# Kernel tuning notes

Hardware: AMD Instinct MI355X
Metric: run time of the kernel (lower is better)

Reference implementation:

```python
import jax, jax.numpy as jnp
import numpy as np

B, N, E = 64, 256, 2048          # graphs per batch, nodes per subgraph, edges per subgraph
V, D, H = 50000, 128, 4          # vocab_size, hidden_dim, heads
NEG_SLOPE = 0.2                  # PyG GATConv default LeakyReLU slope


def setup_inputs() -> dict:
    key = jax.random.key(0)
    ks = jax.random.split(key, 16)
    s = 0.05
    return {
        "neighbors_node1": jax.random.randint(ks[0], (B, N), 0, V),
        "neighbors_node2": jax.random.randint(ks[1], (B, N), 0, V),
        "adj1": jax.random.randint(ks[2], (B, 2, E), 0, N),
        "adj2": jax.random.randint(ks[3], (B, 2, E), 0, N),
        "emb": jax.random.normal(ks[4], (V + 1, D), jnp.float32) * 0.02,
        # GATConv 1: lin weight [H*D, D], att_src/att_dst [H, D], bias [D] (concat=False)
        "W1": jax.random.normal(ks[5], (H * D, D), jnp.float32) * s,
        "att_src1": jax.random.normal(ks[6], (H, D), jnp.float32) * s,
        "att_dst1": jax.random.normal(ks[7], (H, D), jnp.float32) * s,
        "b1": jnp.zeros((D,), jnp.float32),
        # GATConv 2
        "W2": jax.random.normal(ks[8], (H * D, D), jnp.float32) * s,
        "att_src2": jax.random.normal(ks[9], (H, D), jnp.float32) * s,
        "att_dst2": jax.random.normal(ks[10], (H, D), jnp.float32) * s,
        "b2": jnp.zeros((D,), jnp.float32),
        # final MLP: Linear(2D -> 1)
        "mlp_w": jax.random.normal(ks[11], (1, 2 * D), jnp.float32) * s,
        "mlp_b": jnp.zeros((1,), jnp.float32),
    }


def _gat_conv(x, edge_index, W, a_src, a_dst, bias):
    """PyG GATConv, concat=False (mean over heads), with self-loops.
    x: [N, D] node features; edge_index: [2, E] (row=src j, col=dst i)."""
    xh = (x @ W.T).reshape(N, H, D)                      # [N, H, D]
    loop = jnp.arange(N)
    src = jnp.concatenate([edge_index[0], loop])          # [E+N]
    dst = jnp.concatenate([edge_index[1], loop])
    asrc = jnp.einsum('nhd,hd->nh', xh, a_src)            # [N, H]
    adst = jnp.einsum('nhd,hd->nh', xh, a_dst)
    e = jax.nn.leaky_relu(asrc[src] + adst[dst], NEG_SLOPE)   # [E+N, H]
    # softmax over incoming edges of each dst node
    m = jax.ops.segment_max(e, dst, num_segments=N)
    ex = jnp.exp(e - m[dst])
    denom = jax.ops.segment_sum(ex, dst, num_segments=N)
    alpha = ex / denom[dst]                               # [E+N, H]
    out = jax.ops.segment_sum(xh[src] * alpha[:, :, None], dst, num_segments=N)  # [N, H, D]
    return out.mean(axis=1) + bias                        # [N, D]


def reference(neighbors_node1, neighbors_node2, adj1, adj2, emb,
              W1, att_src1, att_dst1, b1,
              W2, att_src2, att_dst2, b2,
              mlp_w, mlp_b):
    f1 = jax.vmap(lambda n, ei: _gat_conv(emb[n], ei, W1, att_src1, att_dst1, b1))(
        neighbors_node1, adj1)                            # [B, N, D]
    f2 = jax.vmap(lambda n, ei: _gat_conv(emb[n], ei, W2, att_src2, att_dst2, b2))(
        neighbors_node2, adj2)
    feats = jnp.concatenate([f1[:, 0], f2[:, 0]], axis=-1)  # center node of each subgraph -> [B, 2D]
    return (feats @ mlp_w.T + mlp_b)[:, 0]                # [B]
```

## Files before the change

kernel.cpp:

```cpp
#include <hip/hip_runtime.h>
#include <hip/hip_bf16.h>

#define Bg 64
#define Nn 256
#define Ee 2048
#define Dd 128
#define Hh 4
#define MAXJ 40
#define RS 132
#define MAGIC 0x13579BDF

__device__ __forceinline__ float loadf(const void* p, long i, int f32) {
    return f32 ? ((const float*)p)[i]
               : __bfloat162float(((const __hip_bfloat16*)p)[i]);
}

__global__ __launch_bounds__(256) void gat_one_kernel(
    const int* nn1, const int* nn2, const int* adj1, const int* adj2,
    const void* emb,
    const void* W1, const void* as1, const void* ad1, const void* b1,
    const void* W2, const void* as2, const void* ad2, const void* b2,
    const void* mlpw, const void* mlpb,
    float* wv,
    int* wvflag,
    float* partial,
    int* pairflag,
    void* out)
{
    __shared__ float s_av[Dd];
    __shared__ float s_wv[12 * RS];
    __shared__ float s_rows[MAXJ * RS];
    __shared__ int   s_srcj[MAXJ];
    __shared__ int   s_gid[MAXJ];
    __shared__ int   s_cnt, s_f32;
    __shared__ float s_ps[MAXJ * Hh], s_pm[MAXJ * Hh];
    __shared__ float s_pd[Hh], s_hval[Hh], s_bd;

    const int tid = threadIdx.x;
    const int x = blockIdx.x;
    const int b = x & (Bg - 1);
    const int l = x >> 6;

    if (tid == 0) { s_f32 = 0; s_cnt = 0; }
    __syncthreads();
    {
        float v = __bfloat162float(((const __hip_bfloat16*)W1)[tid]);
        if (!(v > -64.f && v < 64.f)) atomicOr(&s_f32, 1);
    }
    __syncthreads();
    const int f32 = s_f32;

    if (x < 24) {
        const int h = x & 3, t = (x >> 2) % 3, pl = x / 12;
        const void* avp; long off;
        if (t == 0)      { avp = pl ? as2 : as1; off = (long)h * Dd; }
        else if (t == 1) { avp = pl ? ad2 : ad1; off = (long)h * Dd; }
        else             { avp = mlpw;           off = (long)pl * Dd; }
        if (tid < Dd) s_av[tid] = loadf(avp, off + tid, f32);
        __syncthreads();
        if (tid < Dd) {
            const void* W = pl ? W2 : W1;
            float acc = 0.f;
            if (f32) {
                const float* Wf = (const float*)W + (long)h * Dd * Dd + tid;
                #pragma unroll 8
                for (int d = 0; d < Dd; ++d) acc += s_av[d] * Wf[(long)d * Dd];
            } else {
                const __hip_bfloat16* Wb =
                    (const __hip_bfloat16*)W + (long)h * Dd * Dd + tid;
                #pragma unroll 8
                for (int d = 0; d < Dd; ++d)
                    acc += s_av[d] * __bfloat162float(Wb[(long)d * Dd]);
            }
            __hip_atomic_store(&wv[x * Dd + tid], acc,
                               __ATOMIC_RELAXED, __HIP_MEMORY_SCOPE_AGENT);
        }
        __threadfence();
        __syncthreads();
        if (tid == 0) atomicExch(&wvflag[x], MAGIC);
    } else if (x == 24 || x == 25) {
        const int pl = x - 24;
        if (tid < Dd)
            s_av[tid] = loadf(pl ? b2 : b1, tid, f32) *
                        loadf(mlpw, (long)pl * Dd + tid, f32);
        __syncthreads();
        if (tid == 0) {
            float a = 0.f;
            for (int d = 0; d < Dd; ++d) a += s_av[d];
            if (pl == 0) a += loadf(mlpb, 0, f32);
            __hip_atomic_store(&wv[3072 + pl], a,
                               __ATOMIC_RELAXED, __HIP_MEMORY_SCOPE_AGENT);
            __threadfence();
            atomicExch(&wvflag[24 + pl], MAGIC);
        }
    }

    const int* adjp = (l ? adj2 : adj1) + (long)b * 2 * Ee;
    const int* dstp = adjp + Ee;
    for (int i = tid; i < Ee / 4; i += 256) {
        int4 d4 = ((const int4*)dstp)[i];
        int base = i * 4;
        if (d4.x == 0) { int p = atomicAdd(&s_cnt, 1); if (p < MAXJ - 1) s_srcj[p] = adjp[base + 0]; }
        if (d4.y == 0) { int p = atomicAdd(&s_cnt, 1); if (p < MAXJ - 1) s_srcj[p] = adjp[base + 1]; }
        if (d4.z == 0) { int p = atomicAdd(&s_cnt, 1); if (p < MAXJ - 1) s_srcj[p] = adjp[base + 2]; }
        if (d4.w == 0) { int p = atomicAdd(&s_cnt, 1); if (p < MAXJ - 1) s_srcj[p] = adjp[base + 3]; }
    }
    __syncthreads();
    if (tid == 0) {
        int c = s_cnt; if (c > MAXJ - 1) c = MAXJ - 1;
        s_srcj[c] = 0;
        s_cnt = c + 1;
    }
    __syncthreads();
    const int cnt = s_cnt;

    const int* nodes = l ? nn2 : nn1;
    if (tid < cnt) s_gid[tid] = nodes[b * Nn + s_srcj[tid]];
    __syncthreads();

    for (int idx = tid; idx < cnt * 32; idx += 256) {
        int j = idx >> 5, k4 = (idx & 31) * 4;
        long gid = s_gid[j];
        float4 f;
        if (f32) {
            f = ((const float4*)emb)[gid * 32 + (k4 >> 2)];
        } else {
            const __hip_bfloat16* e = (const __hip_bfloat16*)emb + gid * Dd + k4;
            f.x = __bfloat162float(e[0]); f.y = __bfloat162float(e[1]);
            f.z = __bfloat162float(e[2]); f.w = __bfloat162float(e[3]);
        }
        *(float4*)&s_rows[j * RS + k4] = f;
    }

    if (tid < 13) {
        int fi = (tid < 12) ? (l * 12 + tid) : (24 + l);
        while (__hip_atomic_load(&wvflag[fi], __ATOMIC_ACQUIRE,
                                 __HIP_MEMORY_SCOPE_AGENT) != MAGIC)
            __builtin_amdgcn_s_sleep(1);
    }
    __syncthreads();

    for (int i = tid; i < 12 * Dd; i += 256) {
        int row = i >> 7, k = i & 127;
        s_wv[row * RS + k] = __hip_atomic_load(&wv[(l * 12 + row) * Dd + k],
                                               __ATOMIC_RELAXED,
                                               __HIP_MEMORY_SCOPE_AGENT);
    }
    if (tid == 0)
        s_bd = __hip_atomic_load(&wv[3072 + l], __ATOMIC_RELAXED,
                                 __HIP_MEMORY_SCOPE_AGENT);
    __syncthreads();

    const int ntask = cnt * 8 + Hh;
    for (int task = tid; task < ntask; task += 256) {
        int j, h, t;
        if (task < cnt * 8) {
            j = task >> 3; h = (task >> 1) & 3; t = (task & 1) ? 2 : 0;
        } else {
            h = task - cnt * 8; t = 1; j = cnt - 1;
        }
        const float* wrow = s_wv + (t * 4 + h) * RS;
        const float* row  = s_rows + j * RS;
        float acc = 0.f;
        #pragma unroll 8
        for (int k = 0; k < Dd; ++k) acc += row[k] * wrow[k];
        if (task < cnt * 8) {
            if (task & 1) s_pm[j * Hh + h] = acc;
            else          s_ps[j * Hh + h] = acc;
        } else {
            s_pd[h] = acc;
        }
    }
    __syncthreads();

    if (tid < Hh) {
        float pd = s_pd[tid], m = -1e30f;
        for (int j = 0; j < cnt; ++j) {
            float e = s_ps[j * Hh + tid] + pd;
            e = (e >= 0.f) ? e : 0.2f * e;
            s_ps[j * Hh + tid] = e;
            if (e > m) m = e;
        }
        float den = 0.f, num = 0.f;
        for (int j = 0; j < cnt; ++j) {
            float ex = expf(s_ps[j * Hh + tid] - m);
            den += ex;
            num += ex * s_pm[j * Hh + tid];
        }
        s_hval[tid] = num / den;
    }
    __syncthreads();

    if (tid == 0) {
        float r = 0.25f * (s_hval[0] + s_hval[1] + s_hval[2] + s_hval[3]) + s_bd;
        __hip_atomic_store(&partial[l * Bg + b], r,
                           __ATOMIC_RELAXED, __HIP_MEMORY_SCOPE_AGENT);
        __threadfence();
        int old = atomicExch(&pairflag[b], MAGIC);
        if (old == MAGIC) {
            __threadfence();
            float o = __hip_atomic_load(&partial[(1 - l) * Bg + b],
                                        __ATOMIC_RELAXED,
                                        __HIP_MEMORY_SCOPE_AGENT);
            float vout = r + o;
            if (f32) ((float*)out)[b] = vout;
            else     ((__hip_bfloat16*)out)[b] = __float2bfloat16(vout);
        }
    }
}

extern "C" void kernel_launch(void* const* d_in, const int* in_sizes, int n_in,
                              void* d_out, int out_size, void* d_ws, size_t ws_size,
                              hipStream_t stream) {
    const int* nn1  = (const int*)d_in[0];
    const int* nn2  = (const int*)d_in[1];
    const int* adj1 = (const int*)d_in[2];
    const int* adj2 = (const int*)d_in[3];

    float* ws_f     = (float*)d_ws;
    float* wv       = ws_f;
    int*   wvflag   = (int*)(ws_f + 3074);
    float* partial  = ws_f + 3100;
    int*   pairflag = (int*)(ws_f + 3228);

    gat_one_kernel<<<2 * Bg, 256, 0, stream>>>(
        nn1, nn2, adj1, adj2,
        d_in[4],
        d_in[5],   d_in[6],   d_in[7],
        d_in[8],
        d_in[9],   d_in[10],  d_in[11],
        d_in[12],
        d_in[13],  d_in[14],
        wv, wvflag, partial, pairflag, d_out);
}
```

Baseline: 119.5 us.

## Replace flag-based spin synchronization with cooperative grid sync

Swaps the magic-flag spin waits and the pairwise atomic exchange for a cooperative launch with two grid-wide barriers. The weight-projection blocks now split the 128-long dot product across all 256 threads with a shared-memory combine, and bf16 loads use bit shifts and vectorized ushort4 reads. It also removes the atomic loads when reading back the projected vectors. The trade-off is that every block waits at full-grid barriers, where before each block waited only on the flags it needed.

```diff
diff --git a/kernel.cpp b/kernel.cpp
--- a/kernel.cpp
+++ b/kernel.cpp
@@ -1,5 +1,8 @@
 #include <hip/hip_runtime.h>
+#include <hip/hip_cooperative_groups.h>
 #include <hip/hip_bf16.h>
+
+namespace cg = cooperative_groups;
 
 #define Bg 64
 #define Nn 256
@@ -8,26 +11,25 @@
 #define Hh 4
 #define MAXJ 40
 #define RS 132
-#define MAGIC 0x13579BDF
-
-__device__ __forceinline__ float loadf(const void* p, long i, int f32) {
-    return f32 ? ((const float*)p)[i]
-               : __bfloat162float(((const __hip_bfloat16*)p)[i]);
+
+__device__ __forceinline__ float bf2f(unsigned short u) {
+    return __uint_as_float(((unsigned)u) << 16);
 }
 
-__global__ __launch_bounds__(256) void gat_one_kernel(
+__global__ __launch_bounds__(256) void gat_coop_kernel(
     const int* nn1, const int* nn2, const int* adj1, const int* adj2,
     const void* emb,
     const void* W1, const void* as1, const void* ad1, const void* b1,
     const void* W2, const void* as2, const void* ad2, const void* b2,
     const void* mlpw, const void* mlpb,
-    float* wv,
-    int* wvflag,
+    float* wvg,
     float* partial,
-    int* pairflag,
     void* out)
 {
+    cg::grid_group grid = cg::this_grid();
+
     __shared__ float s_av[Dd];
+    __shared__ float s_half[256];
     __shared__ float s_wv[12 * RS];
     __shared__ float s_rows[MAXJ * RS];
     __shared__ int   s_srcj[MAXJ];
@@ -51,47 +53,57 @@
     const int f32 = s_f32;
 
     if (x < 24) {
-        const int h = x & 3, t = (x >> 2) % 3, pl = x / 12;
+        const int pl = x / 12;
+        const int t  = (x % 12) >> 2;
+        const int h  = x & 3;
         const void* avp; long off;
         if (t == 0)      { avp = pl ? as2 : as1; off = (long)h * Dd; }
         else if (t == 1) { avp = pl ? ad2 : ad1; off = (long)h * Dd; }
         else             { avp = mlpw;           off = (long)pl * Dd; }
-        if (tid < Dd) s_av[tid] = loadf(avp, off + tid, f32);
+        if (tid < Dd)
+            s_av[tid] = f32 ? ((const float*)avp)[off + tid]
+                            : bf2f(((const unsigned short*)avp)[off + tid]);
         __syncthreads();
-        if (tid < Dd) {
-            const void* W = pl ? W2 : W1;
+        {
+            const int k  = tid & 127;
+            const int d0 = (tid >> 7) * 64;
             float acc = 0.f;
             if (f32) {
-                const float* Wf = (const float*)W + (long)h * Dd * Dd + tid;
+                const float* Wf = (const float*)(pl ? W2 : W1)
+                                + ((long)h * Dd + d0) * Dd + k;
                 #pragma unroll 8
-                for (int d = 0; d < Dd; ++d) acc += s_av[d] * Wf[(long)d * Dd];
+                for (int d = 0; d < 64; ++d) acc += s_av[d0 + d] * Wf[(long)d * Dd];
             } else {
-                const __hip_bfloat16* Wb =
-                    (const __hip_bfloat16*)W + (long)h * Dd * Dd + tid;
+                const unsigned short* Wb = (const unsigned short*)(pl ? W2 : W1)
+                                         + ((long)h * Dd + d0) * Dd + k;
                 #pragma unroll 8
-                for (int d = 0; d < Dd; ++d)
-                    acc += s_av[d] * __bfloat162float(Wb[(long)d * Dd]);
+                for (int d = 0; d < 64; ++d) acc += s_av[d0 + d] * bf2f(Wb[(long)d * Dd]);
             }
-            __hip_atomic_store(&wv[x * Dd + tid], acc,
-                               __ATOMIC_RELAXED, __HIP_MEMORY_SCOPE_AGENT);
-        }
-        __threadfence();
+            s_half[tid] = acc;
+        }
         __syncthreads();
-        if (tid == 0) atomicExch(&wvflag[x], MAGIC);
-    } else if (x == 24 || x == 25) {
+        if (tid < Dd) wvg[x * Dd + tid] = s_half[tid] + s_half[tid + 128];
+    } else if (x < 26) {
         const int pl = x - 24;
-        if (tid < Dd)
-            s_av[tid] = loadf(pl ? b2 : b1, tid, f32) *
-                        loadf(mlpw, (long)pl * Dd + tid, f32);
+        if (tid < Dd) {
+            const void* bias = pl ? b2 : b1;
+            float bv = f32 ? ((const float*)bias)[tid]
+                           : bf2f(((const unsigned short*)bias)[tid]);
+            float mv = f32 ? ((const float*)mlpw)[pl * Dd + tid]
+                           : bf2f(((const unsigned short*)mlpw)[pl * Dd + tid]);
+            s_half[tid] = bv * mv;
+        }
         __syncthreads();
+        for (int s = 64; s > 0; s >>= 1) {
+            if (tid < s) s_half[tid] += s_half[tid + s];
+            __syncthreads();
+        }
         if (tid == 0) {
-            float a = 0.f;
-            for (int d = 0; d < Dd; ++d) a += s_av[d];
-            if (pl == 0) a += loadf(mlpb, 0, f32);
-            __hip_atomic_store(&wv[3072 + pl], a,
-                               __ATOMIC_RELAXED, __HIP_MEMORY_SCOPE_AGENT);
-            __threadfence();
-            atomicExch(&wvflag[24 + pl], MAGIC);
+            float a = s_half[0];
+            if (pl == 0)
+                a += f32 ? ((const float*)mlpb)[0]
+                         : bf2f(((const unsigned short*)mlpb)[0]);
+            wvg[3072 + pl] = a;
         }
     }
 
@@ -113,11 +125,9 @@
     }
     __syncthreads();
     const int cnt = s_cnt;
-
     const int* nodes = l ? nn2 : nn1;
     if (tid < cnt) s_gid[tid] = nodes[b * Nn + s_srcj[tid]];
     __syncthreads();
-
     for (int idx = tid; idx < cnt * 32; idx += 256) {
         int j = idx >> 5, k4 = (idx & 31) * 4;
         long gid = s_gid[j];
@@ -125,30 +135,20 @@
         if (f32) {
             f = ((const float4*)emb)[gid * 32 + (k4 >> 2)];
         } else {
-            const __hip_bfloat16* e = (const __hip_bfloat16*)emb + gid * Dd + k4;
-            f.x = __bfloat162float(e[0]); f.y = __bfloat162float(e[1]);
-            f.z = __bfloat162float(e[2]); f.w = __bfloat162float(e[3]);
+            ushort4 u = *(const ushort4*)((const unsigned short*)emb + gid * Dd + k4);
+            f.x = bf2f(u.x); f.y = bf2f(u.y); f.z = bf2f(u.z); f.w = bf2f(u.w);
         }
         *(float4*)&s_rows[j * RS + k4] = f;
     }
 
-    if (tid < 13) {
-        int fi = (tid < 12) ? (l * 12 + tid) : (24 + l);
-        while (__hip_atomic_load(&wvflag[fi], __ATOMIC_ACQUIRE,
-                                 __HIP_MEMORY_SCOPE_AGENT) != MAGIC)
-            __builtin_amdgcn_s_sleep(1);
-    }
-    __syncthreads();
-
-    for (int i = tid; i < 12 * Dd; i += 256) {
-        int row = i >> 7, k = i & 127;
-        s_wv[row * RS + k] = __hip_atomic_load(&wv[(l * 12 + row) * Dd + k],
-                                               __ATOMIC_RELAXED,
-                                               __HIP_MEMORY_SCOPE_AGENT);
-    }
-    if (tid == 0)
-        s_bd = __hip_atomic_load(&wv[3072 + l], __ATOMIC_RELAXED,
-                                 __HIP_MEMORY_SCOPE_AGENT);
+    grid.sync();
+
+    for (int i = tid; i < 12 * Dd / 4; i += 256) {
+        float4 f = ((const float4*)(wvg + l * 12 * Dd))[i];
+        int el = i * 4, row = el >> 7, k = el & 127;
+        *(float4*)&s_wv[row * RS + k] = f;
+    }
+    if (tid == 0) s_bd = wvg[3072 + l];
     __syncthreads();
 
     const int ntask = cnt * 8 + Hh;
@@ -190,22 +190,15 @@
         s_hval[tid] = num / den;
     }
     __syncthreads();
-
-    if (tid == 0) {
-        float r = 0.25f * (s_hval[0] + s_hval[1] + s_hval[2] + s_hval[3]) + s_bd;
-        __hip_atomic_store(&partial[l * Bg + b], r,
-                           __ATOMIC_RELAXED, __HIP_MEMORY_SCOPE_AGENT);
-        __threadfence();
-        int old = atomicExch(&pairflag[b], MAGIC);
-        if (old == MAGIC) {
-            __threadfence();
-            float o = __hip_atomic_load(&partial[(1 - l) * Bg + b],
-                                        __ATOMIC_RELAXED,
-                                        __HIP_MEMORY_SCOPE_AGENT);
-            float vout = r + o;
-            if (f32) ((float*)out)[b] = vout;
-            else     ((__hip_bfloat16*)out)[b] = __float2bfloat16(vout);
-        }
+    if (tid == 0)
+        partial[x] = 0.25f * (s_hval[0] + s_hval[1] + s_hval[2] + s_hval[3]) + s_bd;
+
+    grid.sync();
+
+    if (x < Bg && tid == 0) {
+        float r = partial[b] + partial[Bg + b];
+        if (f32) ((float*)out)[b] = r;
+        else     ((__hip_bfloat16*)out)[b] = __float2bfloat16(r);
     }
 }
 
@@ -216,20 +209,30 @@
     const int* nn2  = (const int*)d_in[1];
     const int* adj1 = (const int*)d_in[2];
     const int* adj2 = (const int*)d_in[3];
-
-    float* ws_f     = (float*)d_ws;
-    float* wv       = ws_f;
-    int*   wvflag   = (int*)(ws_f + 3074);
-    float* partial  = ws_f + 3100;
-    int*   pairflag = (int*)(ws_f + 3228);
-
-    gat_one_kernel<<<2 * Bg, 256, 0, stream>>>(
-        nn1, nn2, adj1, adj2,
-        d_in[4],
-        d_in[5],   d_in[6],   d_in[7],
-        d_in[8],
-        d_in[9],   d_in[10],  d_in[11],
-        d_in[12],
-        d_in[13],  d_in[14],
-        wv, wvflag, partial, pairflag, d_out);
+    const void* emb  = d_in[4];
+    const void* W1   = d_in[5];
+    const void* as1  = d_in[6];
+    const void* ad1  = d_in[7];
+    const void* b1   = d_in[8];
+    const void* W2   = d_in[9];
+    const void* as2  = d_in[10];
+    const void* ad2  = d_in[11];
+    const void* b2   = d_in[12];
+    const void* mlpw = d_in[13];
+    const void* mlpb = d_in[14];
+
+    float* wvg     = (float*)d_ws;
+    float* partial = wvg + 3074;
+    void*  out     = d_out;
+
+    void* args[] = {
+        (void*)&nn1, (void*)&nn2, (void*)&adj1, (void*)&adj2,
+        (void*)&emb,
+        (void*)&W1, (void*)&as1, (void*)&ad1, (void*)&b1,
+        (void*)&W2, (void*)&as2, (void*)&ad2, (void*)&b2,
+        (void*)&mlpw, (void*)&mlpb,
+        (void*)&wvg, (void*)&partial, (void*)&out
+    };
+    hipLaunchCooperativeKernel((const void*)gat_coop_kernel,
+                               dim3(2 * Bg), dim3(256), args, 0, stream);
 }
```

New measurement: 169.2 us. +41.7%, slower.
